# Kernel optimization log

Hardware: AMD Instinct MI355X
Metric: run time of the kernel (lower is better)

Reference implementation:

```python
import jax, jax.numpy as jnp
import numpy as np

N, C, H, W = 16, 128, 64, 64
SHIFT = 1  # fixed value of the init-time random.randint(-2, 2)
DN = ('NCHW', 'OIHW', 'NCHW')


def setup_inputs() -> dict:
    key = jax.random.key(0)
    ks = jax.random.split(key, 6)
    x = jax.random.normal(ks[0], (N, C, H, W), jnp.float32)
    p2 = jax.random.normal(ks[1], (1, C, 1, 1, W), jnp.float32) * 0.1   # trunc_normal std=0.1
    p3 = jax.random.normal(ks[2], (1, C, 7, 1, 1), jnp.float32) * 0.1
    p4 = jax.random.normal(ks[3], (1, C, H, W), jnp.float32) * 0.1
    w6 = jax.random.normal(ks[4], (C, 1, 3, 1), jnp.float32) * 0.1      # depthwise (3,1), dil (3,1)
    w7 = jax.random.normal(ks[5], (C * 7, C, 1, 7), jnp.float32) * 0.05 # dense (1,7)
    return {'x': x, 'p2': p2, 'p3': p3, 'p4': p4, 'w6': w6, 'w7': w7}


def reference(x, p2, p3, p4, w6, w7):
    n, c, h, w = x.shape
    # F.unfold(x, (7,1), dilation=(2,1), padding=(6,0)) -> (n, c, 7, h, w)
    xp = jnp.pad(x, ((0, 0), (0, 0), (6, 6), (0, 0)))
    t1 = jnp.stack([xp[:, :, 2 * k:2 * k + h, :] for k in range(7)], axis=2)
    t3 = p3 * (p2 * t1)                                   # fused gating multiplies
    t5 = jnp.roll(p4 * x, SHIFT, axis=3)
    t6 = jax.lax.conv_general_dilated(t5, w6, (1, 1), ((3, 3), (0, 0)),
                                      rhs_dilation=(3, 1), dimension_numbers=DN,
                                      feature_group_count=c)             # (n,c,h,w)
    t7 = jax.lax.conv_general_dilated(x, w7, (1, 1), ((0, 0), (3, 3)),
                                      dimension_numbers=DN)              # (n,7c,h,w)
    s = h * w
    t8 = jnp.einsum('ncs,nks->nck', x.reshape(n, c, s),
                    t3.reshape(n, c * 7, s)) / float(np.sqrt(s))         # (n,c,7c)
    t9 = jnp.einsum('nck,nks->ncs', t8,
                    t7.reshape(n, c * 7, s)) / float(np.sqrt(c * 7))
    return t9.reshape(n, c, h, w) - t6
```

## Files before the change

### kernel.cpp

```cpp
#include <hip/hip_runtime.h>

#define NB 16
#define CD 128
#define HD 64
#define WD 64
#define SD 4096
#define K7 896
#define XROW 72

typedef float  f32x4  __attribute__((ext_vector_type(4)));
typedef __bf16 bf16x8 __attribute__((ext_vector_type(8)));
typedef __bf16 bf16x4 __attribute__((ext_vector_type(4)));

typedef __attribute__((address_space(3))) void lds_void_t;
typedef const __attribute__((address_space(1))) void gbl_void_t;

__device__ __forceinline__ void gl16(const void* g, void* l) {
  __builtin_amdgcn_global_load_lds((gbl_void_t*)g, (lds_void_t*)l, 16, 0, 0);
}

__global__ __launch_bounds__(256)
void cvt_ximg(const float* __restrict__ x, __bf16* __restrict__ ximg) {
  const int idx = (blockIdx.x * 256 + threadIdx.x) * 8;
  const float4 a = *(const float4*)(x + idx);
  const float4 b = *(const float4*)(x + idx + 4);
  bf16x8 v;
  v[0] = (__bf16)a.x; v[1] = (__bf16)a.y; v[2] = (__bf16)a.z; v[3] = (__bf16)a.w;
  v[4] = (__bf16)b.x; v[5] = (__bf16)b.y; v[6] = (__bf16)b.z; v[7] = (__bf16)b.w;
  const int plane = idx >> 12;
  const int n = plane >> 7, c = plane & 127;
  const int s0 = idx & 4095;
  const int stepg = s0 >> 5, kg = (s0 >> 3) & 3;
  *(bf16x8*)(ximg + ((size_t)((n * 128 + stepg) * 4 + kg) * 128 + c) * 8) = v;
}

__global__ __launch_bounds__(256)
void w7img_kernel(const float* __restrict__ w7, const float* __restrict__ p3,
                  __bf16* __restrict__ w7img) {
  __shared__ float tile[64][65];
  const int b2 = blockIdx.x * 64;
  const int bp = blockIdx.y * 64;
  const int t  = threadIdx.x;
  const int col = t & 63;
  const int r0  = t >> 6;
#pragma unroll
  for (int rr = 0; rr < 16; ++rr) {
    const int row = rr * 4 + r0;
    tile[col][row] = w7[(size_t)(bp + row) * K7 + b2 + col];
  }
  __syncthreads();
  const int kpr = bp + col;
  const float p3v = p3[kpr];
#pragma unroll
  for (int rr = 0; rr < 16; ++rr) {
    const int row = rr * 4 + r0;
    const int k2  = b2 + row;
    const int c2  = k2 / 7, q = k2 - c2 * 7;
    const int k2q = q * 128 + c2;
    const size_t off = ((size_t)((k2q >> 6) * 28 + (kpr >> 5)) * 4 + ((kpr >> 3) & 3)) * 512
                     + (k2q & 63) * 8 + (kpr & 7);
    w7img[off] = (__bf16)(tile[row][col] * p3v);
  }
}

__global__ __launch_bounds__(256)
void xt_kernel(const float* __restrict__ x, __bf16* __restrict__ xT) {
  __shared__ __bf16 tile[128][72];
  const int n = blockIdx.y;
  const int i = blockIdx.x;
  const int t = threadIdx.x;
  const float* src = x + (size_t)n * CD * SD + (size_t)i * WD;
#pragma unroll
  for (int it = 0; it < 4; ++it) {
    const int c = it * 32 + (t >> 3);
    const int j = (t & 7) * 8;
    const float* s2 = src + (size_t)c * SD + j;
    const float4 a = *(const float4*)s2;
    const float4 b = *(const float4*)(s2 + 4);
    bf16x8 v;
    v[0] = (__bf16)a.x; v[1] = (__bf16)a.y; v[2] = (__bf16)a.z; v[3] = (__bf16)a.w;
    v[4] = (__bf16)b.x; v[5] = (__bf16)b.y; v[6] = (__bf16)b.z; v[7] = (__bf16)b.w;
    *(bf16x8*)&tile[c][j] = v;
  }
  __bf16* dstn = xT + ((size_t)n * HD + i) * XROW * CD;
  if (t < 128) {
    const int pr = t >> 4;
    const int rowz = pr < 3 ? pr : 64 + pr;
    bf16x8 z = {};
    *(bf16x8*)(dstn + (size_t)rowz * CD + (t & 15) * 8) = z;
  }
  __syncthreads();
#pragma unroll
  for (int it = 0; it < 4; ++it) {
    const int j   = t >> 2;
    const int c2b = (t & 3) * 32 + it * 8;
    bf16x8 v;
#pragma unroll
    for (int e = 0; e < 8; ++e) v[e] = tile[c2b + e][j];
    *(bf16x8*)(dstn + (size_t)(j + 3) * CD + c2b) = v;
  }
}

__global__ __launch_bounds__(256)
void p4t_kernel(const float* __restrict__ p4, __bf16* __restrict__ p4T) {
  __shared__ __bf16 tile[128][72];
  const int i = blockIdx.x;
  const int t = threadIdx.x;
#pragma unroll
  for (int it = 0; it < 4; ++it) {
    const int c = it * 32 + (t >> 3);
    const int j = (t & 7) * 8;
    const float* src = p4 + (size_t)c * SD + (size_t)i * WD + j;
    const float4 a = *(const float4*)src;
    const float4 b = *(const float4*)(src + 4);
    bf16x8 v;
    v[0] = (__bf16)a.x; v[1] = (__bf16)a.y; v[2] = (__bf16)a.z; v[3] = (__bf16)a.w;
    v[4] = (__bf16)b.x; v[5] = (__bf16)b.y; v[6] = (__bf16)b.z; v[7] = (__bf16)b.w;
    *(bf16x8*)&tile[c][j] = v;
  }
  __bf16* dst = p4T + (size_t)i * XROW * CD;
  if (t < 128) {
    const int pr = t >> 4;
    const int rowz = pr < 3 ? pr : 64 + pr;
    bf16x8 z = {};
    *(bf16x8*)(dst + (size_t)rowz * CD + (t & 15) * 8) = z;
  }
  __syncthreads();
#pragma unroll
  for (int it = 0; it < 4; ++it) {
    const int j   = t >> 2;
    const int c2b = (t & 3) * 32 + it * 8;
    bf16x8 v;
#pragma unroll
    for (int e = 0; e < 8; ++e) v[e] = tile[c2b + e][j];
    *(bf16x8*)(dst + (size_t)(j + 3) * CD + c2b) = v;
  }
}

template<int KC>
__global__ __launch_bounds__(256)
void reduce_img(const __bf16* __restrict__ part, __bf16* __restrict__ img,
                float scale) {
  const int idx8 = blockIdx.x * 256 + threadIdx.x;
  const int r = idx8 / 112;
  const int kchunk = idx8 - r * 112;
  const size_t in = (size_t)r * K7 + kchunk * 8;
  const size_t stride = (size_t)NB * CD * K7;
  float s[8];
  bf16x8 v = *(const bf16x8*)(part + in);
#pragma unroll
  for (int e = 0; e < 8; ++e) s[e] = (float)v[e];
#pragma unroll
  for (int c = 1; c < KC; ++c) {
    bf16x8 p = *(const bf16x8*)(part + c * stride + in);
#pragma unroll
    for (int e = 0; e < 8; ++e) s[e] += (float)p[e];
  }
  bf16x8 o;
#pragma unroll
  for (int e = 0; e < 8; ++e) o[e] = (__bf16)(s[e] * scale);
  const size_t out = ((size_t)(((r >> 7) * 28 + (kchunk >> 2)) * 4 + (kchunk & 3)) * 128
                      + (r & 127)) * 8;
  *(bf16x8*)(img + out) = o;
}

#define COMPUTE_STD(AB, BB)                                                     \
  do {                                                                          \
    bf16x8 af[4], bfr[2];                                                       \
    _Pragma("unroll")                                                           \
    for (int fm = 0; fm < 4; ++fm)                                              \
      af[fm] = *(const bf16x8*)&As[AB][(lg * 128 + wm * 64 + fm * 16 + l16) * 8]; \
    _Pragma("unroll")                                                           \
    for (int fn = 0; fn < 2; ++fn)                                              \
      bfr[fn] = *(const bf16x8*)&Bs[BB][(lg * 64 + wn * 32 + fn * 16 + l16) * 8]; \
    _Pragma("unroll")                                                           \
    for (int fm = 0; fm < 4; ++fm)                                              \
      _Pragma("unroll")                                                         \
      for (int fn = 0; fn < 2; ++fn)                                            \
        acc[fm][fn] = __builtin_amdgcn_mfma_f32_16x16x32_bf16(af[fm], bfr[fn],  \
                                                              acc[fm][fn], 0, 0, 0); \
  } while (0)

#define COMPUTE_SWZ(AB, BB, H)                                                  \
  do {                                                                          \
    bf16x8 af[4], bfr[2];                                                       \
    const int swz = ((((H) * 4 + lg) ^ (l16 & 7)) * 8);                         \
    _Pragma("unroll")                                                           \
    for (int fm = 0; fm < 4; ++fm)                                              \
      af[fm] = *(const bf16x8*)&As[AB][(lg * 128 + wm * 64 + fm * 16 + l16) * 8]; \
    _Pragma("unroll")                                                           \
    for (int fn = 0; fn < 2; ++fn)                                              \
      bfr[fn] = *(const bf16x8*)&Bs[BB][(wn * 32 + fn * 16 + l16) * 64 + swz];  \
    _Pragma("unroll")                                                           \
    for (int fm = 0; fm < 4; ++fm)                                              \
      _Pragma("unroll")                                                         \
      for (int fn = 0; fn < 2; ++fn)                                            \
        acc[fm][fn] = __builtin_amdgcn_mfma_f32_16x16x32_bf16(af[fm], bfr[fn],  \
                                                              acc[fm][fn], 0, 0, 0); \
  } while (0)

__global__ __launch_bounds__(256)
void t8_mfma(const float* __restrict__ x, const __bf16* __restrict__ ximg,
             const float* __restrict__ p2, __bf16* __restrict__ part) {
  __shared__ __bf16 As[2][4096];
  __shared__ __bf16 Bs[2][4096];
  const int b = blockIdx.x;
  const int xcd = b & 7, slot = b >> 3;
  const int n  = xcd * 2 + slot / 56;
  const int r56 = slot % 56;
  const int kc = r56 / 14;
  const int n0 = (r56 % 14) * 64;
  const int t = threadIdx.x;
  const int lane = t & 63, wid = t >> 6;
  const int wm = wid & 1, wn = wid >> 1;
  const int l16 = lane & 15, lg = lane >> 4;
  const int wb = wid * 512;

  const __bf16* aptr = ximg + ((size_t)(n * 128 + kc * 32) * 512 + t) * 8;

  const int rw1 = wid * 16 + (lane >> 3);
  const int rw2 = rw1 + 8;
  const int kp1 = n0 + rw1, kp2 = n0 + rw2;
  const int c21 = kp1 / 7, kk1 = kp1 - c21 * 7;
  const int c22 = kp2 / 7, kk2 = kp2 - c22 * 7;
  const int scd = (lane & 7) ^ ((lane >> 3) & 7);
  const float* xr1 = x + ((size_t)n * CD + c21) * SD + scd * 8;
  const float* xr2 = x + ((size_t)n * CD + c22) * SD + scd * 8;
  float g1[8], g2[8];
#pragma unroll
  for (int e = 0; e < 8; ++e) {
    g1[e] = p2[c21 * WD + scd * 8 + e];
    g2[e] = p2[c22 * WD + scd * 8 + e];
  }
  const int d1 = rw1 * 64 + (lane & 7) * 8;
  const int d2 = d1 + 512;

  f32x4 acc[4][2] = {};
  const int P = 16;

  float4 u10, u11, u20, u21;
  bool v1, v2;

#define T8A(B, ST) do {                                            \
    gl16(aptr + (size_t)(ST) * 4096,        &As[B][wb]);           \
    gl16(aptr + (size_t)(ST) * 4096 + 2048, &As[B][wb + 2048]);    \
  } while (0)
#define T8B_LOAD(PP) do {                                          \
    const int i_ = kc * 16 + (PP);                                 \
    const int ip1 = i_ + 2 * kk1 - 6, ip2 = i_ + 2 * kk2 - 6;      \
    v1 = ((unsigned)ip1 < (unsigned)HD);                           \
    v2 = ((unsigned)ip2 < (unsigned)HD);                           \
    if (v1) { u10 = *(const float4*)(xr1 + ip1 * 64);              \
              u11 = *(const float4*)(xr1 + ip1 * 64 + 4); }        \
    if (v2) { u20 = *(const float4*)(xr2 + ip2 * 64);              \
              u21 = *(const float4*)(xr2 + ip2 * 64 + 4); }        \
  } while (0)
#define T8B_WRITE(B) do {                                          \
    bf16x8 b1 = {}, b2 = {};                                       \
    if (v1) {                                                      \
      b1[0]=(__bf16)(u10.x*g1[0]); b1[1]=(__bf16)(u10.y*g1[1]);    \
      b1[2]=(__bf16)(u10.z*g1[2]); b1[3]=(__bf16)(u10.w*g1[3]);    \
      b1[4]=(__bf16)(u11.x*g1[4]); b1[5]=(__bf16)(u11.y*g1[5]);    \
      b1[6]=(__bf16)(u11.z*g1[6]); b1[7]=(__bf16)(u11.w*g1[7]);    \
    }                                                              \
    if (v2) {                                                      \
      b2[0]=(__bf16)(u20.x*g2[0]); b2[1]=(__bf16)(u20.y*g2[1]);    \
      b2[2]=(__bf16)(u20.z*g2[2]); b2[3]=(__bf16)(u20.w*g2[3]);    \
      b2[4]=(__bf16)(u21.x*g2[4]); b2[5]=(__bf16)(u21.y*g2[5]);    \
      b2[6]=(__bf16)(u21.z*g2[6]); b2[7]=(__bf16)(u21.w*g2[7]);    \
    }                                                              \
    *(bf16x8*)&Bs[B][d1] = b1;                                     \
    *(bf16x8*)&Bs[B][d2] = b2;                                     \
  } while (0)

  T8B_LOAD(0);
  T8A(0, 0);
  T8B_WRITE(0);
  __syncthreads();
  for (int p = 0; p < P; ++p) {
    const int pb = p & 1;
    if (p + 1 < P) T8B_LOAD(p + 1);
    T8A(1, 2 * p + 1);
    COMPUTE_SWZ(0, pb, 0);
    if (p + 1 < P) T8B_WRITE(pb ^ 1);
    __syncthreads();
    if (p + 1 < P) T8A(0, 2 * p + 2);
    COMPUTE_SWZ(1, pb, 1);
    __syncthreads();
  }
#undef T8A
#undef T8B_LOAD
#undef T8B_WRITE

  const int colb = n0 + wn * 32 + l16;
  __bf16* pb2 = part + ((size_t)(kc * NB + n) * CD) * K7;
#pragma unroll
  for (int fm = 0; fm < 4; ++fm)
#pragma unroll
    for (int r = 0; r < 4; ++r) {
      const int c1 = wm * 64 + fm * 16 + lg * 4 + r;
      __bf16* orow = pb2 + (size_t)c1 * K7 + colb;
      orow[0]  = (__bf16)acc[fm][0][r];
      orow[16] = (__bf16)acc[fm][1][r];
    }
}

__global__ __launch_bounds__(256)
void m_mfma(const __bf16* __restrict__ t8img, const __bf16* __restrict__ w7img,
            __bf16* __restrict__ part) {
  __shared__ __bf16 As[2][4096];
  __shared__ __bf16 Bs[2][2048];
  const int tile = blockIdx.x;
  const int n    = blockIdx.y;
  const int kc   = blockIdx.z;
  const int t = threadIdx.x;
  const int lane = t & 63, wid = t >> 6;
  const int wm = wid & 1, wn = wid >> 1;
  const int l16 = lane & 15, lg = lane >> 4;
  const int wb = wid * 512;

  const __bf16* aptr = t8img + ((size_t)(n * 28 + kc * 14) * 512 + t) * 8;
  const __bf16* bptr = w7img + ((size_t)(tile * 28 + kc * 14) * 256 + t) * 8;

  f32x4 acc[4][2] = {};
  const int NSTEP = 14;

#define M_STG(B, ST) do {                                          \
    gl16(aptr + (size_t)(ST) * 4096,        &As[B][wb]);           \
    gl16(aptr + (size_t)(ST) * 4096 + 2048, &As[B][wb + 2048]);    \
    gl16(bptr + (size_t)(ST) * 2048,        &Bs[B][wb]);           \
  } while (0)

  M_STG(0, 0);
  int cur = 0;
  for (int st = 0; st < NSTEP; ++st) {
    __syncthreads();
    if (st + 1 < NSTEP) M_STG(cur ^ 1, st + 1);
    COMPUTE_STD(cur, cur);
    cur ^= 1;
  }
#undef M_STG

  const int colb = tile * 64 + wn * 32 + l16;
  __bf16* pb = part + (size_t)kc * (NB * CD * K7);
#pragma unroll
  for (int fm = 0; fm < 4; ++fm)
#pragma unroll
    for (int r = 0; r < 4; ++r) {
      const int mr = n * 128 + wm * 64 + fm * 16 + lg * 4 + r;
      __bf16* orow = pb + (size_t)mr * K7 + colb;
      orow[0]  = (__bf16)acc[fm][0][r];
      orow[16] = (__bf16)acc[fm][1][r];
    }
}

__global__ __launch_bounds__(256)
void out_mfma(const __bf16* __restrict__ mimg, const __bf16* __restrict__ xT,
              const __bf16* __restrict__ p4T, const float* __restrict__ w6,
              float* __restrict__ outp) {
  __shared__ __bf16 As[2][4096];
  __shared__ __bf16 Bs[2][4096];
  const int b = blockIdx.x;
  const int xcd = b & 7, slot = b >> 3;
  const int n = (xcd << 1) | (slot >> 6);
  const int i = slot & 63;
  const int t = threadIdx.x;
  const int lane = t & 63, wid = t >> 6;
  const int wm = wid & 1, wn = wid >> 1;
  const int l16 = lane & 15, lg = lane >> 4;
  const int wb = wid * 512;

  const __bf16* aptr = mimg + ((size_t)n * 28 * 512 + t) * 8;

  const int colw = wid * 16 + (lane >> 3);
  const int scd8 = ((lane & 7) ^ ((lane >> 3) & 7)) * 8;
  const __bf16* bptr1 = xT + (((size_t)n * HD + i) * XROW + colw) * CD + scd8;
  const __bf16* bptr2 = bptr1 + 8 * CD;

  f32x4 acc[4][2] = {};
  const int P = 14;

#define OA(B, ST) do {                                             \
    gl16(aptr + (size_t)(ST) * 4096,        &As[B][wb]);           \
    gl16(aptr + (size_t)(ST) * 4096 + 2048, &As[B][wb + 2048]);    \
  } while (0)
#define OB(B, PP) do {                                             \
    gl16(bptr1 + (PP) * 64, &Bs[B][wid * 1024]);                   \
    gl16(bptr2 + (PP) * 64, &Bs[B][wid * 1024 + 512]);             \
  } while (0)

  OA(0, 0);
  OB(0, 0);
  __syncthreads();
  for (int p = 0; p < P; ++p) {
    const int pb = p & 1;
    if (p + 1 < P) OB(pb ^ 1, p + 1);
    OA(1, 2 * p + 1);
    COMPUTE_SWZ(0, pb, 0);
    __syncthreads();
    if (p + 1 < P) OA(0, 2 * p + 2);
    COMPUTE_SWZ(1, pb, 1);
    __syncthreads();
  }
#undef OA
#undef OB

  const __bf16* xTn = xT + (size_t)n * HD * XROW * CD;
#pragma unroll
  for (int fm = 0; fm < 4; ++fm) {
    const int cbase = wm * 64 + fm * 16 + lg * 4;
    const float4 wa  = *(const float4*)(w6 + cbase * 3);
    const float4 wbv = *(const float4*)(w6 + cbase * 3 + 4);
    const float4 wc  = *(const float4*)(w6 + cbase * 3 + 8);
    const float w6v[4][3] = {{wa.x, wa.y, wa.z}, {wa.w, wbv.x, wbv.y},
                             {wbv.z, wbv.w, wc.x}, {wc.y, wc.z, wc.w}};
#pragma unroll
    for (int fn = 0; fn < 2; ++fn) {
      const int j  = wn * 32 + fn * 16 + l16;
      const int jm = (j - 1) & 63;
      const size_t ro = (size_t)(jm + 3) * CD + cbase;
      float t6v[4] = {0.f, 0.f, 0.f, 0.f};
#pragma unroll
      for (int rr = 0; rr < 3; ++rr) {
        const int ip = i + 3 * rr - 3;
        if ((unsigned)ip < (unsigned)HD) {
          const bf16x4 xv = *(const bf16x4*)(xTn + (size_t)ip * XROW * CD + ro);
          const bf16x4 pv = *(const bf16x4*)(p4T + (size_t)ip * XROW * CD + ro);
#pragma unroll
          for (int rq = 0; rq < 4; ++rq)
            t6v[rq] += w6v[rq][rr] * (float)pv[rq] * (float)xv[rq];
        }
      }
      float* obase = outp + ((size_t)(n * CD + cbase)) * SD + i * WD + j;
#pragma unroll
      for (int rq = 0; rq < 4; ++rq)
        obase[(size_t)rq * SD] = acc[fm][fn][rq] - t6v[rq];
    }
  }
}

extern "C" void kernel_launch(void* const* d_in, const int* in_sizes, int n_in,
                              void* d_out, int out_size, void* d_ws, size_t ws_size,
                              hipStream_t stream) {
  const float* x  = (const float*)d_in[0];
  const float* p2 = (const float*)d_in[1];
  const float* p3 = (const float*)d_in[2];
  const float* p4 = (const float*)d_in[3];
  const float* w6 = (const float*)d_in[4];
  const float* w7 = (const float*)d_in[5];
  float* outp = (float*)d_out;

  const size_t e_x   = (size_t)NB * CD * SD;
  const size_t e_t8  = (size_t)NB * CD * K7;
  const size_t e_w7  = (size_t)K7 * K7;
  const size_t e_xT  = (size_t)NB * HD * XROW * CD;
  const size_t e_p4T = (size_t)HD * XROW * CD;

  __bf16* ximg  = (__bf16*)d_ws;
  __bf16* t8img = ximg + e_x;
  __bf16* mimg  = t8img + e_t8;
  __bf16* w7img = mimg + e_t8;
  __bf16* region = w7img + e_w7;
  __bf16* partT8 = region;
  __bf16* partM  = region;
  __bf16* xT   = region;
  __bf16* p4T  = region + e_xT;

  dim3 blk(256);
  cvt_ximg<<<dim3((unsigned)(e_x / 2048)), blk, 0, stream>>>(x, ximg);
  w7img_kernel<<<dim3(14, 14), blk, 0, stream>>>(w7, p3, w7img);

  t8_mfma<<<dim3(896), blk, 0, stream>>>(x, ximg, p2, partT8);
  reduce_img<4><<<dim3(896), blk, 0, stream>>>(partT8, t8img, 1.f / 64.f);

  m_mfma<<<dim3(14, 16, 2), blk, 0, stream>>>(t8img, w7img, partM);
  reduce_img<2><<<dim3(896), blk, 0, stream>>>(partM, mimg, 0.033407655f);

  xt_kernel<<<dim3(HD, NB), blk, 0, stream>>>(x, xT);
  p4t_kernel<<<dim3(HD), blk, 0, stream>>>(p4, p4T);
  out_mfma<<<dim3(1024), blk, 0, stream>>>(mimg, xT, p4T, w6, outp);
}
```

Baseline: 150.1 us.

## Precompute padded x*p2 bf16 planes and deepen GEMM pipelines to four stages

Adds a pre-padded bf16 buffer holding x*p2, written during the x conversion kernel with a separate kernel zeroing the pad rows. When the workspace is large enough, the t8 GEMM stages its B operand straight from that buffer with async global-to-LDS loads, instead of gathering fp32 x and multiplying by p2 in registers. All three MFMA GEMMs now use a 4-buffer ring with explicit vmcnt waits and barriers, so up to three stages of loads are in flight. The cost is extra workspace, one extra kernel launch, more LDS per block (which may reduce occupancy), and a smaller B tile layout with a new swizzle.

After: 160.5 us. 1.07x slower.

```diff
diff --git a/kernel.cpp b/kernel.cpp
--- a/kernel.cpp
+++ b/kernel.cpp
@@ -7,6 +7,7 @@
 #define SD 4096
 #define K7 896
 #define XROW 72
+#define SD2 4864
 
 typedef float  f32x4  __attribute__((ext_vector_type(4)));
 typedef __bf16 bf16x8 __attribute__((ext_vector_type(8)));
@@ -19,8 +20,17 @@
   __builtin_amdgcn_global_load_lds((gbl_void_t*)g, (lds_void_t*)l, 16, 0, 0);
 }
 
-__global__ __launch_bounds__(256)
-void cvt_ximg(const float* __restrict__ x, __bf16* __restrict__ ximg) {
+template<int N>
+__device__ __forceinline__ void wbar() {
+  __builtin_amdgcn_sched_barrier(0);
+  asm volatile("s_waitcnt vmcnt(%0)" :: "i"(N) : "memory");
+  __builtin_amdgcn_s_barrier();
+  __builtin_amdgcn_sched_barrier(0);
+}
+
+__global__ __launch_bounds__(256)
+void cvt_ximg(const float* __restrict__ x, const float* __restrict__ p2,
+              __bf16* __restrict__ ximg, __bf16* __restrict__ xp2) {
   const int idx = (blockIdx.x * 256 + threadIdx.x) * 8;
   const float4 a = *(const float4*)(x + idx);
   const float4 b = *(const float4*)(x + idx + 4);
@@ -32,6 +42,27 @@
   const int s0 = idx & 4095;
   const int stepg = s0 >> 5, kg = (s0 >> 3) & 3;
   *(bf16x8*)(ximg + ((size_t)((n * 128 + stepg) * 4 + kg) * 128 + c) * 8) = v;
+  if (xp2) {
+    const int j = s0 & 63;
+    const float4 pa = *(const float4*)(p2 + c * 64 + j);
+    const float4 pb = *(const float4*)(p2 + c * 64 + j + 4);
+    bf16x8 w;
+    w[0] = (__bf16)(a.x * pa.x); w[1] = (__bf16)(a.y * pa.y);
+    w[2] = (__bf16)(a.z * pa.z); w[3] = (__bf16)(a.w * pa.w);
+    w[4] = (__bf16)(b.x * pb.x); w[5] = (__bf16)(b.y * pb.y);
+    w[6] = (__bf16)(b.z * pb.z); w[7] = (__bf16)(b.w * pb.w);
+    *(bf16x8*)(xp2 + (size_t)plane * SD2 + 384 + s0) = w;
+  }
+}
+
+__global__ __launch_bounds__(256)
+void pad0_kernel(__bf16* __restrict__ xp2) {
+  const int u = (blockIdx.x * 256 + threadIdx.x) * 8;
+  const int plane = u / 768;
+  const int r = u - plane * 768;
+  const int off = (r < 384) ? r : (r + 4096);
+  bf16x8 z = {};
+  *(bf16x8*)(xp2 + (size_t)plane * SD2 + off) = z;
 }
 
 __global__ __launch_bounds__(256)
@@ -181,16 +212,17 @@
                                                               acc[fm][fn], 0, 0, 0); \
   } while (0)
 
-#define COMPUTE_SWZ(AB, BB, H)                                                  \
+#define COMPUTE_SWZB(AB, BB)                                                    \
   do {                                                                          \
     bf16x8 af[4], bfr[2];                                                       \
-    const int swz = ((((H) * 4 + lg) ^ (l16 & 7)) * 8);                         \
     _Pragma("unroll")                                                           \
     for (int fm = 0; fm < 4; ++fm)                                              \
       af[fm] = *(const bf16x8*)&As[AB][(lg * 128 + wm * 64 + fm * 16 + l16) * 8]; \
     _Pragma("unroll")                                                           \
-    for (int fn = 0; fn < 2; ++fn)                                              \
-      bfr[fn] = *(const bf16x8*)&Bs[BB][(wn * 32 + fn * 16 + l16) * 64 + swz];  \
+    for (int fn = 0; fn < 2; ++fn) {                                            \
+      const int rc = wn * 32 + fn * 16 + l16;                                   \
+      bfr[fn] = *(const bf16x8*)&Bs[BB][(rc * 4 + (lg ^ (rc & 3))) * 8];        \
+    }                                                                           \
     _Pragma("unroll")                                                           \
     for (int fm = 0; fm < 4; ++fm)                                              \
       _Pragma("unroll")                                                         \
@@ -199,11 +231,32 @@
                                                               acc[fm][fn], 0, 0, 0); \
   } while (0)
 
+#define COMPUTE_SWZ(AB, BB, H)                                                  \
+  do {                                                                          \
+    bf16x8 af[4], bfr[2];                                                       \
+    const int swz = ((((H) * 4 + lg) ^ (l16 & 7)) * 8);                         \
+    _Pragma("unroll")                                                           \
+    for (int fm = 0; fm < 4; ++fm)                                              \
+      af[fm] = *(const bf16x8*)&As[AB][(lg * 128 + wm * 64 + fm * 16 + l16) * 8]; \
+    _Pragma("unroll")                                                           \
+    for (int fn = 0; fn < 2; ++fn)                                              \
+      bfr[fn] = *(const bf16x8*)&Bs[BB][(wn * 32 + fn * 16 + l16) * 64 + swz];  \
+    _Pragma("unroll")                                                           \
+    for (int fm = 0; fm < 4; ++fm)                                              \
+      _Pragma("unroll")                                                         \
+      for (int fn = 0; fn < 2; ++fn)                                            \
+        acc[fm][fn] = __builtin_amdgcn_mfma_f32_16x16x32_bf16(af[fm], bfr[fn],  \
+                                                              acc[fm][fn], 0, 0, 0); \
+  } while (0)
+
+template<bool XP2>
 __global__ __launch_bounds__(256)
 void t8_mfma(const float* __restrict__ x, const __bf16* __restrict__ ximg,
-             const float* __restrict__ p2, __bf16* __restrict__ part) {
-  __shared__ __bf16 As[2][4096];
-  __shared__ __bf16 Bs[2][4096];
+             const __bf16* __restrict__ xp2, const float* __restrict__ p2,
+             __bf16* __restrict__ part) {
+  constexpr int NA = XP2 ? 4 : 2;
+  __shared__ __bf16 As[NA][4096];
+  __shared__ __bf16 Bs[NA][XP2 ? 2048 : 4096];
   const int b = blockIdx.x;
   const int xcd = b & 7, slot = b >> 3;
   const int n  = xcd * 2 + slot / 56;
@@ -218,29 +271,53 @@
 
   const __bf16* aptr = ximg + ((size_t)(n * 128 + kc * 32) * 512 + t) * 8;
 
-  const int rw1 = wid * 16 + (lane >> 3);
-  const int rw2 = rw1 + 8;
-  const int kp1 = n0 + rw1, kp2 = n0 + rw2;
-  const int c21 = kp1 / 7, kk1 = kp1 - c21 * 7;
-  const int c22 = kp2 / 7, kk2 = kp2 - c22 * 7;
-  const int scd = (lane & 7) ^ ((lane >> 3) & 7);
-  const float* xr1 = x + ((size_t)n * CD + c21) * SD + scd * 8;
-  const float* xr2 = x + ((size_t)n * CD + c22) * SD + scd * 8;
-  float g1[8], g2[8];
-#pragma unroll
-  for (int e = 0; e < 8; ++e) {
-    g1[e] = p2[c21 * WD + scd * 8 + e];
-    g2[e] = p2[c22 * WD + scd * 8 + e];
-  }
-  const int d1 = rw1 * 64 + (lane & 7) * 8;
-  const int d2 = d1 + 512;
-
   f32x4 acc[4][2] = {};
-  const int P = 16;
-
-  float4 u10, u11, u20, u21;
-  bool v1, v2;
-
+  const int NSTEP = 32;
+
+  if constexpr (XP2) {
+    const int rl = lane >> 2;
+    const int r  = wid * 16 + rl;
+    const int kp = n0 + r;
+    const int c2 = kp / 7, kk = kp - c2 * 7;
+    const int kgd = (lane & 3) ^ (rl & 3);
+    const __bf16* bptr = xp2 + ((size_t)(n * 128 + c2) * 76 + kc * 16 + 2 * kk) * 64
+                       + kgd * 8;
+
+#define T8_STG(B, ST) do {                                         \
+    gl16(aptr + (size_t)(ST) * 4096,        &As[B][wb]);           \
+    gl16(aptr + (size_t)(ST) * 4096 + 2048, &As[B][wb + 2048]);    \
+    gl16(bptr + (ST) * 32,                  &Bs[B][wb]);           \
+  } while (0)
+
+    T8_STG(0, 0); T8_STG(1, 1); T8_STG(2, 2);
+    for (int st = 0; st < NSTEP - 2; ++st) {
+      wbar<6>();
+      if (st + 3 < NSTEP) T8_STG((st + 3) & 3, st + 3);
+      COMPUTE_SWZB(st & 3, st & 3);
+    }
+    wbar<3>(); COMPUTE_SWZB((NSTEP - 2) & 3, (NSTEP - 2) & 3);
+    wbar<0>(); COMPUTE_SWZB((NSTEP - 1) & 3, (NSTEP - 1) & 3);
+#undef T8_STG
+  } else {
+    const int rw1 = wid * 16 + (lane >> 3);
+    const int rw2 = rw1 + 8;
+    const int kp1 = n0 + rw1, kp2 = n0 + rw2;
+    const int c21 = kp1 / 7, kk1 = kp1 - c21 * 7;
+    const int c22 = kp2 / 7, kk2 = kp2 - c22 * 7;
+    const int scd = (lane & 7) ^ ((lane >> 3) & 7);
+    const float* xr1 = x + ((size_t)n * CD + c21) * SD + scd * 8;
+    const float* xr2 = x + ((size_t)n * CD + c22) * SD + scd * 8;
+    float g1[8], g2[8];
+#pragma unroll
+    for (int e = 0; e < 8; ++e) {
+      g1[e] = p2[c21 * WD + scd * 8 + e];
+      g2[e] = p2[c22 * WD + scd * 8 + e];
+    }
+    const int d1 = rw1 * 64 + (lane & 7) * 8;
+    const int d2 = d1 + 512;
+    const int P = 16;
+    float4 u10, u11, u20, u21;
+    bool v1, v2;
 #define T8A(B, ST) do {                                            \
     gl16(aptr + (size_t)(ST) * 4096,        &As[B][wb]);           \
     gl16(aptr + (size_t)(ST) * 4096 + 2048, &As[B][wb + 2048]);    \
@@ -272,44 +349,44 @@
     *(bf16x8*)&Bs[B][d1] = b1;                                     \
     *(bf16x8*)&Bs[B][d2] = b2;                                     \
   } while (0)
-
-  T8B_LOAD(0);
-  T8A(0, 0);
-  T8B_WRITE(0);
-  __syncthreads();
-  for (int p = 0; p < P; ++p) {
-    const int pb = p & 1;
-    if (p + 1 < P) T8B_LOAD(p + 1);
-    T8A(1, 2 * p + 1);
-    COMPUTE_SWZ(0, pb, 0);
-    if (p + 1 < P) T8B_WRITE(pb ^ 1);
+    T8B_LOAD(0);
+    T8A(0, 0);
+    T8B_WRITE(0);
     __syncthreads();
-    if (p + 1 < P) T8A(0, 2 * p + 2);
-    COMPUTE_SWZ(1, pb, 1);
-    __syncthreads();
-  }
+    for (int p = 0; p < P; ++p) {
+      const int pb = p & 1;
+      if (p + 1 < P) T8B_LOAD(p + 1);
+      T8A(1, 2 * p + 1);
+      COMPUTE_SWZ(0, pb, 0);
+      if (p + 1 < P) T8B_WRITE(pb ^ 1);
+      __syncthreads();
+      if (p + 1 < P) T8A(0, 2 * p + 2);
+      COMPUTE_SWZ(1, pb, 1);
+      __syncthreads();
+    }
 #undef T8A
 #undef T8B_LOAD
 #undef T8B_WRITE
+  }
 
   const int colb = n0 + wn * 32 + l16;
   __bf16* pb2 = part + ((size_t)(kc * NB + n) * CD) * K7;
 #pragma unroll
   for (int fm = 0; fm < 4; ++fm)
 #pragma unroll
-    for (int r = 0; r < 4; ++r) {
-      const int c1 = wm * 64 + fm * 16 + lg * 4 + r;
+    for (int r2 = 0; r2 < 4; ++r2) {
+      const int c1 = wm * 64 + fm * 16 + lg * 4 + r2;
       __bf16* orow = pb2 + (size_t)c1 * K7 + colb;
-      orow[0]  = (__bf16)acc[fm][0][r];
-      orow[16] = (__bf16)acc[fm][1][r];
+      orow[0]  = (__bf16)acc[fm][0][r2];
+      orow[16] = (__bf16)acc[fm][1][r2];
     }
 }
 
 __global__ __launch_bounds__(256)
 void m_mfma(const __bf16* __restrict__ t8img, const __bf16* __restrict__ w7img,
             __bf16* __restrict__ part) {
-  __shared__ __bf16 As[2][4096];
-  __shared__ __bf16 Bs[2][2048];
+  __shared__ __bf16 As[4][4096];
+  __shared__ __bf16 Bs[4][2048];
   const int tile = blockIdx.x;
   const int n    = blockIdx.y;
   const int kc   = blockIdx.z;
@@ -331,14 +408,14 @@
     gl16(bptr + (size_t)(ST) * 2048,        &Bs[B][wb]);           \
   } while (0)
 
-  M_STG(0, 0);
-  int cur = 0;
-  for (int st = 0; st < NSTEP; ++st) {
-    __syncthreads();
-    if (st + 1 < NSTEP) M_STG(cur ^ 1, st + 1);
-    COMPUTE_STD(cur, cur);
-    cur ^= 1;
-  }
+  M_STG(0, 0); M_STG(1, 1); M_STG(2, 2);
+  for (int st = 0; st < NSTEP - 2; ++st) {
+    wbar<6>();
+    if (st + 3 < NSTEP) M_STG((st + 3) & 3, st + 3);
+    COMPUTE_STD(st & 3, st & 3);
+  }
+  wbar<3>(); COMPUTE_STD((NSTEP - 2) & 3, (NSTEP - 2) & 3);
+  wbar<0>(); COMPUTE_STD((NSTEP - 1) & 3, (NSTEP - 1) & 3);
 #undef M_STG
 
   const int colb = tile * 64 + wn * 32 + l16;
@@ -358,8 +435,8 @@
 void out_mfma(const __bf16* __restrict__ mimg, const __bf16* __restrict__ xT,
               const __bf16* __restrict__ p4T, const float* __restrict__ w6,
               float* __restrict__ outp) {
-  __shared__ __bf16 As[2][4096];
-  __shared__ __bf16 Bs[2][4096];
+  __shared__ __bf16 As[4][4096];
+  __shared__ __bf16 Bs[4][2048];
   const int b = blockIdx.x;
   const int xcd = b & 7, slot = b >> 3;
   const int n = (xcd << 1) | (slot >> 6);
@@ -372,38 +449,29 @@
 
   const __bf16* aptr = mimg + ((size_t)n * 28 * 512 + t) * 8;
 
-  const int colw = wid * 16 + (lane >> 3);
-  const int scd8 = ((lane & 7) ^ ((lane >> 3) & 7)) * 8;
-  const __bf16* bptr1 = xT + (((size_t)n * HD + i) * XROW + colw) * CD + scd8;
-  const __bf16* bptr2 = bptr1 + 8 * CD;
+  const int jl = lane >> 2;
+  const int j  = wid * 16 + jl;
+  const int kgd = (lane & 3) ^ (jl & 3);
+  const __bf16* bptr = xT + (((size_t)(n * HD + i)) * XROW + j) * CD + kgd * 8;
 
   f32x4 acc[4][2] = {};
-  const int P = 14;
-
-#define OA(B, ST) do {                                             \
+  const int NSTEP = 28;
+
+#define O_STG(B, ST) do {                                          \
     gl16(aptr + (size_t)(ST) * 4096,        &As[B][wb]);           \
     gl16(aptr + (size_t)(ST) * 4096 + 2048, &As[B][wb + 2048]);    \
-  } while (0)
-#define OB(B, PP) do {                                             \
-    gl16(bptr1 + (PP) * 64, &Bs[B][wid * 1024]);                   \
-    gl16(bptr2 + (PP) * 64, &Bs[B][wid * 1024 + 512]);             \
-  } while (0)
-
-  OA(0, 0);
-  OB(0, 0);
-  __syncthreads();
-  for (int p = 0; p < P; ++p) {
-    const int pb = p & 1;
-    if (p + 1 < P) OB(pb ^ 1, p + 1);
-    OA(1, 2 * p + 1);
-    COMPUTE_SWZ(0, pb, 0);
-    __syncthreads();
-    if (p + 1 < P) OA(0, 2 * p + 2);
-    COMPUTE_SWZ(1, pb, 1);
-    __syncthreads();
-  }
-#undef OA
-#undef OB
+    gl16(bptr + (ST) * 32,                  &Bs[B][wb]);           \
+  } while (0)
+
+  O_STG(0, 0); O_STG(1, 1); O_STG(2, 2);
+  for (int st = 0; st < NSTEP - 2; ++st) {
+    wbar<6>();
+    if (st + 3 < NSTEP) O_STG((st + 3) & 3, st + 3);
+    COMPUTE_SWZB(st & 3, st & 3);
+  }
+  wbar<3>(); COMPUTE_SWZB((NSTEP - 2) & 3, (NSTEP - 2) & 3);
+  wbar<0>(); COMPUTE_SWZB((NSTEP - 1) & 3, (NSTEP - 1) & 3);
+#undef O_STG
 
   const __bf16* xTn = xT + (size_t)n * HD * XROW * CD;
 #pragma unroll
@@ -416,8 +484,8 @@
                              {wbv.z, wbv.w, wc.x}, {wc.y, wc.z, wc.w}};
 #pragma unroll
     for (int fn = 0; fn < 2; ++fn) {
-      const int j  = wn * 32 + fn * 16 + l16;
-      const int jm = (j - 1) & 63;
+      const int jj = wn * 32 + fn * 16 + l16;
+      const int jm = (jj - 1) & 63;
       const size_t ro = (size_t)(jm + 3) * CD + cbase;
       float t6v[4] = {0.f, 0.f, 0.f, 0.f};
 #pragma unroll
@@ -431,7 +499,7 @@
             t6v[rq] += w6v[rq][rr] * (float)pv[rq] * (float)xv[rq];
         }
       }
-      float* obase = outp + ((size_t)(n * CD + cbase)) * SD + i * WD + j;
+      float* obase = outp + ((size_t)(n * CD + cbase)) * SD + i * WD + jj;
 #pragma unroll
       for (int rq = 0; rq < 4; ++rq)
         obase[(size_t)rq * SD] = acc[fm][fn][rq] - t6v[rq];
@@ -453,24 +521,35 @@
   const size_t e_x   = (size_t)NB * CD * SD;
   const size_t e_t8  = (size_t)NB * CD * K7;
   const size_t e_w7  = (size_t)K7 * K7;
+  const size_t e_xp2 = (size_t)NB * CD * SD2;
   const size_t e_xT  = (size_t)NB * HD * XROW * CD;
   const size_t e_p4T = (size_t)HD * XROW * CD;
+
+  const size_t base_b = (e_x + 2 * e_t8 + e_w7) * 2;
+  const size_t xp2_b  = (e_xp2 + 4 * e_t8) * 2;
+  const bool   tierA  = ws_size >= base_b + xp2_b;
 
   __bf16* ximg  = (__bf16*)d_ws;
   __bf16* t8img = ximg + e_x;
   __bf16* mimg  = t8img + e_t8;
   __bf16* w7img = mimg + e_t8;
   __bf16* region = w7img + e_w7;
-  __bf16* partT8 = region;
+  __bf16* xp2    = tierA ? region : nullptr;
+  __bf16* partT8 = tierA ? (region + e_xp2) : region;
   __bf16* partM  = region;
-  __bf16* xT   = region;
-  __bf16* p4T  = region + e_xT;
+  __bf16* xT     = region;
+  __bf16* p4T    = region + e_xT;
 
   dim3 blk(256);
-  cvt_ximg<<<dim3((unsigned)(e_x / 2048)), blk, 0, stream>>>(x, ximg);
+  cvt_ximg<<<dim3((unsigned)(e_x / 2048)), blk, 0, stream>>>(x, p2, ximg, xp2);
+  if (tierA)
+    pad0_kernel<<<dim3((unsigned)(NB * CD * 768 / 2048)), blk, 0, stream>>>(xp2);
   w7img_kernel<<<dim3(14, 14), blk, 0, stream>>>(w7, p3, w7img);
 
-  t8_mfma<<<dim3(896), blk, 0, stream>>>(x, ximg, p2, partT8);
+  if (tierA)
+    t8_mfma<true><<<dim3(896), blk, 0, stream>>>(x, ximg, xp2, p2, partT8);
+  else
+    t8_mfma<false><<<dim3(896), blk, 0, stream>>>(x, ximg, nullptr, p2, partT8);
   reduce_img<4><<<dim3(896), blk, 0, stream>>>(partT8, t8img, 1.f / 64.f);
 
   m_mfma<<<dim3(14, 16, 2), blk, 0, stream>>>(t8img, w7img, partM);
```
